# Kernel optimization log

Hardware: AMD Instinct MI355X
Metric: run time of the kernel (lower is better)

Reference implementation:

```python
import jax, jax.numpy as jnp
import numpy as np

NORM = 1.0  # normalization_factor


def _glorot(key, shape):
    fan_in, fan_out = shape
    lim = float(np.sqrt(6.0 / (fan_in + fan_out)))
    return jax.random.uniform(key, shape, jnp.float32, -lim, lim)


def setup_inputs() -> dict:
    key = jax.random.key(0)
    ks = jax.random.split(key, 12)
    B, N = 8, 2048
    latent, hidden, out_dim = 64, 128, 64
    inp = {
        "latent_features": jax.random.normal(ks[0], (B, N, latent), jnp.float32),
        "adjacency_matrix": jax.random.uniform(ks[1], (B, N, N), jnp.float32),
        "node_mask": jnp.ones((B, N, 1), jnp.float32),
        # 3 GCN layers: latent->hidden, hidden->hidden, hidden->hidden
        "W0": _glorot(ks[2], (latent, hidden)), "b0": jnp.zeros((hidden,), jnp.float32),
        "W1": _glorot(ks[3], (hidden, hidden)), "b1": jnp.zeros((hidden,), jnp.float32),
        "W2": _glorot(ks[4], (hidden, hidden)), "b2": jnp.zeros((hidden,), jnp.float32),
        # output projection hidden->out_dim
        "Wout": _glorot(ks[5], (hidden, out_dim)), "bout": jnp.zeros((out_dim,), jnp.float32),
    }
    return inp


def _gcn_layer(h, adj, W, b):
    # message transform (linear), gather+sum aggregate via dense adjacency, ReLU act
    msg = h @ W + b                      # [B,N,dout]
    agg = jnp.einsum('bij,bjd->bid', adj, msg) / NORM  # sum aggregation over neighbors
    return jax.nn.relu(agg)


def reference(latent_features, adjacency_matrix, node_mask,
              W0, b0, W1, b1, W2, b2, Wout, bout):
    h = _gcn_layer(latent_features, adjacency_matrix, W0, b0)
    h = _gcn_layer(h, adjacency_matrix, W1, b1)
    h = _gcn_layer(h, adjacency_matrix, W2, b2)
    # output projection + node mask
    return (h @ Wout + bout) * node_mask
```

## Files before the change

kernel.cpp:

```cpp
#include <hip/hip_runtime.h>
#include <hip/hip_bf16.h>


typedef __bf16 bf16;
typedef __bf16 bf16x4 __attribute__((ext_vector_type(4)));
typedef __bf16 bf16x8 __attribute__((ext_vector_type(8)));
typedef float  f32x16 __attribute__((ext_vector_type(16)));
typedef float  f32x4  __attribute__((ext_vector_type(4)));

static __device__ inline f32x16 mfma32(bf16x8 a, bf16x8 b, f32x16 c) {
    return __builtin_amdgcn_mfma_f32_32x32x16_bf16(a, b, c, 0, 0, 0);
}

static __device__ inline void tile_barrier() {
    asm volatile("s_waitcnt lgkmcnt(0)" ::: "memory");
    __builtin_amdgcn_s_barrier();
    asm volatile("" ::: "memory");
}

#define NB   8
#define NN   2048
#define LAT  64
#define HID  128
#define ODIM 64

__global__ __launch_bounds__(256) void prep_t0_k(
    const float* __restrict__ lat, const float* __restrict__ W0,
    const float* __restrict__ b0,
    const float* __restrict__ W1, const float* __restrict__ W2,
    const float* __restrict__ Wout,
    bf16* __restrict__ msgT, bf16* __restrict__ WT1,
    bf16* __restrict__ WT2, bf16* __restrict__ WoutT)
{
    __shared__ __align__(16) bf16 WTs[HID * 72];
    int tid = threadIdx.x;
    int blk = blockIdx.x;

    if (blk >= 256) {
        int i = (blk - 256) * 256 + tid;
        if (i < HID * HID) { int fo = i >> 7, k = i & 127; WT1[i] = (bf16)W1[k * HID + fo]; return; }
        i -= HID * HID;
        if (i < HID * HID) { int fo = i >> 7, k = i & 127; WT2[i] = (bf16)W2[k * HID + fo]; return; }
        i -= HID * HID;
        if (i < ODIM * HID) { int o = i >> 7, k = i & 127; WoutT[i] = (bf16)Wout[k * ODIM + o]; return; }
        return;
    }

    for (int i = tid; i < LAT * HID; i += 256) {
        int k = i >> 7, fo = i & 127;
        WTs[fo * 72 + k] = (bf16)W0[i];
    }
    __syncthreads();

    int l = tid & 63, w = tid >> 6;
    int lm = l & 31, lh = l >> 5;
    int g0 = blk * 64;
    int b  = g0 >> 11, nb = g0 & 2047;

    const bf16*  Wrow = &WTs[(w * 32 + lm) * 72 + lh * 8];
    const float* r0   = lat + (size_t)(g0 + lm) * LAT + lh * 8;
    const float* r1   = r0 + (size_t)32 * LAT;

    f32x16 acc0 = {}, acc1 = {};
#pragma unroll
    for (int k0 = 0; k0 < LAT; k0 += 16) {
        bf16x8 a = *(const bf16x8*)(Wrow + k0);
        f32x4 x0 = *(const f32x4*)(r0 + k0), x1 = *(const f32x4*)(r0 + k0 + 4);
        f32x4 y0 = *(const f32x4*)(r1 + k0), y1 = *(const f32x4*)(r1 + k0 + 4);
        bf16x8 v0, v1;
        v0[0]=(bf16)x0[0]; v0[1]=(bf16)x0[1]; v0[2]=(bf16)x0[2]; v0[3]=(bf16)x0[3];
        v0[4]=(bf16)x1[0]; v0[5]=(bf16)x1[1]; v0[6]=(bf16)x1[2]; v0[7]=(bf16)x1[3];
        v1[0]=(bf16)y0[0]; v1[1]=(bf16)y0[1]; v1[2]=(bf16)y0[2]; v1[3]=(bf16)y0[3];
        v1[4]=(bf16)y1[0]; v1[5]=(bf16)y1[1]; v1[6]=(bf16)y1[2]; v1[7]=(bf16)y1[3];
        acc0 = mfma32(a, v0, acc0);
        acc1 = mfma32(a, v1, acc1);
    }

    bf16* outb = msgT + (size_t)b * (HID * NN) + nb;
#pragma unroll
    for (int r = 0; r < 16; ++r) {
        int fo = w * 32 + (r & 3) + 8 * (r >> 2) + 4 * lh;
        float bv = b0[fo];
        outb[(size_t)fo * NN + lm]      = (bf16)(acc0[r] + bv);
        outb[(size_t)fo * NN + 32 + lm] = (bf16)(acc1[r] + bv);
    }
}

template<int MODE, int ADJW>
__global__ __launch_bounds__(256) void agg_k(
    const float* __restrict__ adjf, const bf16* __restrict__ adjbi,
    bf16* __restrict__ adjbo,
    const bf16* __restrict__ msgT, const bf16* __restrict__ WTn,
    const float* __restrict__ biasn, bf16* __restrict__ msg_out,
    const float* __restrict__ mask, float* __restrict__ out)
{
    __shared__ __align__(16) bf16 As[2][32 * 72];
    __shared__ __align__(16) bf16 Bs[2][128 * 72];
    __shared__ __align__(16) bf16 Hs[32 * 136];
    int tid = threadIdx.x;
    int l = tid & 63, w = tid >> 6;
    int lm = l & 31, lh = l >> 5;
    int b  = blockIdx.x & 7;
    int m0 = (blockIdx.x >> 3) * 32;

    const bf16* msgb = msgT + (size_t)b * (HID * NN);
    int br = tid >> 3, bc = (tid & 7) * 8;
    const bf16* bsrc = msgb + (size_t)br * NN + bc;

    int ar = tid >> 4, ac = (tid & 15) * 4;
    const float* asrc = (ADJW == 0) ? adjf + (size_t)b * NN * NN + (size_t)(m0 + ar) * NN + ac : nullptr;
    bf16* adst = (ADJW == 0) ? adjbo + (size_t)b * NN * NN + (size_t)(m0 + ar) * NN + ac : nullptr;
    int ar8 = tid >> 3, ac8 = (tid & 7) * 8;
    const bf16* asrcb = (ADJW == 1) ? adjbi + (size_t)b * NN * NN + (size_t)(m0 + ar8) * NN + ac8 : nullptr;

    f32x4  fa0[2], fa1[2];
    bf16x8 ba[2];
    bf16x8 pb[2][4];

    auto loadTile = [&](int set, int k) {
        if (ADJW == 0) {
            fa0[set] = *(const f32x4*)(asrc + k);
            fa1[set] = *(const f32x4*)(asrc + (size_t)16 * NN + k);
        } else {
            ba[set] = *(const bf16x8*)(asrcb + k);
        }
        pb[set][0] = *(const bf16x8*)(bsrc + k);
        pb[set][1] = *(const bf16x8*)(bsrc + (size_t)32 * NN + k);
        pb[set][2] = *(const bf16x8*)(bsrc + (size_t)64 * NN + k);
        pb[set][3] = *(const bf16x8*)(bsrc + (size_t)96 * NN + k);
    };
    auto storeTile = [&](int set, int buf, int k) {
        if (ADJW == 0) {
            bf16x4 v0, v1;
            v0[0]=(bf16)fa0[set][0]; v0[1]=(bf16)fa0[set][1]; v0[2]=(bf16)fa0[set][2]; v0[3]=(bf16)fa0[set][3];
            v1[0]=(bf16)fa1[set][0]; v1[1]=(bf16)fa1[set][1]; v1[2]=(bf16)fa1[set][2]; v1[3]=(bf16)fa1[set][3];
            *(bf16x4*)&As[buf][ar * 72 + ac]        = v0;
            *(bf16x4*)&As[buf][(ar + 16) * 72 + ac] = v1;
            *(bf16x4*)(adst + k)                    = v0;
            *(bf16x4*)(adst + (size_t)16 * NN + k)  = v1;
        } else {
            *(bf16x8*)&As[buf][ar8 * 72 + ac8] = ba[set];
        }
        *(bf16x8*)&Bs[buf][br * 72 + bc]        = pb[set][0];
        *(bf16x8*)&Bs[buf][(br + 32) * 72 + bc] = pb[set][1];
        *(bf16x8*)&Bs[buf][(br + 64) * 72 + bc] = pb[set][2];
        *(bf16x8*)&Bs[buf][(br + 96) * 72 + bc] = pb[set][3];
    };

    f32x16 acc = {};
    auto mfmaTile = [&](int buf) {
        const bf16* Ac = &As[buf][lm * 72 + lh * 8];
        const bf16* Bc = &Bs[buf][(w * 32 + lm) * 72 + lh * 8];
#pragma unroll
        for (int s = 0; s < 4; ++s)
            acc = mfma32(*(const bf16x8*)(Ac + s * 16), *(const bf16x8*)(Bc + s * 16), acc);
    };

    loadTile(0, 0);
    loadTile(1, 64);
    storeTile(0, 0, 0);
    tile_barrier();

#pragma unroll 1
    for (int kt = 0; kt < 32; kt += 2) {
        if (kt + 2 < 32) loadTile(0, (kt + 2) * 64);
        mfmaTile(0);
        storeTile(1, 1, (kt + 1) * 64);
        tile_barrier();
        if (kt + 3 < 32) loadTile(1, (kt + 3) * 64);
        mfmaTile(1);
        if (kt + 2 < 32) storeTile(0, 0, (kt + 2) * 64);
        tile_barrier();
    }

#pragma unroll
    for (int r = 0; r < 16; ++r) {
        int row = (r & 3) + 8 * (r >> 2) + 4 * lh;
        float v = acc[r];
        Hs[row * 136 + w * 32 + lm] = (bf16)(v > 0.f ? v : 0.f);
    }
    __syncthreads();

    if (MODE == 0) {
        const bf16* Arow = WTn + (size_t)(w * 32 + lm) * HID + lh * 8;
        const bf16* Brow = &Hs[lm * 136 + lh * 8];
        f32x16 acc2 = {};
#pragma unroll
        for (int s = 0; s < 8; ++s)
            acc2 = mfma32(*(const bf16x8*)(Arow + s * 16), *(const bf16x8*)(Brow + s * 16), acc2);
        bf16* outb = msg_out + (size_t)b * (HID * NN) + m0;
#pragma unroll
        for (int r = 0; r < 16; ++r) {
            int fo = w * 32 + (r & 3) + 8 * (r >> 2) + 4 * lh;
            outb[(size_t)fo * NN + lm] = (bf16)(acc2[r] + biasn[fo]);
        }
    } else {
        if (w < 2) {
            int ob = w * 32;
            const bf16* Arow = &Hs[lm * 136 + lh * 8];
            const bf16* Brow = WTn + (size_t)(ob + lm) * HID + lh * 8;
            f32x16 acc2 = {};
#pragma unroll
            for (int s = 0; s < 8; ++s)
                acc2 = mfma32(*(const bf16x8*)(Arow + s * 16), *(const bf16x8*)(Brow + s * 16), acc2);
            float bv = biasn[ob + lm];
#pragma unroll
            for (int r = 0; r < 16; ++r) {
                int node = (r & 3) + 8 * (r >> 2) + 4 * lh;
                int g = b * NN + m0 + node;
                out[(size_t)g * ODIM + ob + lm] = (acc2[r] + bv) * mask[g];
            }
        }
    }
}

extern "C" void kernel_launch(void* const* d_in, const int* in_sizes, int n_in,
                              void* d_out, int out_size, void* d_ws, size_t ws_size,
                              hipStream_t stream)
{
    const float* lat  = (const float*)d_in[0];
    const float* adj  = (const float*)d_in[1];
    const float* mask = (const float*)d_in[2];
    const float* W0   = (const float*)d_in[3];
    const float* b0   = (const float*)d_in[4];
    const float* W1   = (const float*)d_in[5];
    const float* b1   = (const float*)d_in[6];
    const float* W2   = (const float*)d_in[7];
    const float* b2   = (const float*)d_in[8];
    const float* Wout = (const float*)d_in[9];
    const float* bout = (const float*)d_in[10];
    float* out = (float*)d_out;

    char* ws = (char*)d_ws;
    bf16* msgA  = (bf16*)(ws + 0);
    bf16* msgB  = (bf16*)(ws + 4194304);
    bf16* adjbf = (bf16*)(ws + 8388608);
    bf16* WT1   = (bf16*)(ws + 75497472);
    bf16* WT2   = (bf16*)(ws + 75530240);
    bf16* WoutT = (bf16*)(ws + 75563008);

    prep_t0_k<<<416, 256, 0, stream>>>(lat, W0, b0, W1, W2, Wout, msgA, WT1, WT2, WoutT);

    agg_k<0, 0><<<512, 256, 0, stream>>>(adj, nullptr, adjbf, msgA, WT1, b1, msgB, nullptr, nullptr);
    agg_k<0, 1><<<512, 256, 0, stream>>>(nullptr, adjbf, nullptr, msgB, WT2, b2, msgA, nullptr, nullptr);
    agg_k<1, 1><<<512, 256, 0, stream>>>(nullptr, adjbf, nullptr, msgA, WoutT, bout, nullptr, mask, out);
}
```

Before: 284.8 us.

## Enlarge aggregation tiles to 64 rows and 128-deep K with 512-thread blocks

The aggregation kernel now processes 64 output rows per block instead of 32, and takes a K step of 128 instead of 64. It runs 8 waves arranged 2x4 over 256 blocks. This halves how often the msg matrix is re-read from global memory per row block and halves the number of barriers. The store for the next tile is now issued before the MFMAs rather than after. The trade-off is larger LDS use (about 87KB) and fewer blocks than CUs, which could leave some compute units idle.

```diff
diff --git a/kernel.cpp b/kernel.cpp
--- a/kernel.cpp
+++ b/kernel.cpp
@@ -23,6 +23,10 @@
 #define LAT  64
 #define HID  128
 #define ODIM 64
+#define BM   64
+#define BK   128
+#define NP   16
+#define LDK  136
 
 __global__ __launch_bounds__(256) void prep_t0_k(
     const float* __restrict__ lat, const float* __restrict__ W0,
@@ -87,117 +91,128 @@
 }
 
 template<int MODE, int ADJW>
-__global__ __launch_bounds__(256) void agg_k(
+__global__ __launch_bounds__(512) void agg_k(
     const float* __restrict__ adjf, const bf16* __restrict__ adjbi,
     bf16* __restrict__ adjbo,
     const bf16* __restrict__ msgT, const bf16* __restrict__ WTn,
     const float* __restrict__ biasn, bf16* __restrict__ msg_out,
     const float* __restrict__ mask, float* __restrict__ out)
 {
-    __shared__ __align__(16) bf16 As[2][32 * 72];
-    __shared__ __align__(16) bf16 Bs[2][128 * 72];
-    __shared__ __align__(16) bf16 Hs[32 * 136];
+    __shared__ __align__(16) bf16 As[2][BM * LDK];
+    __shared__ __align__(16) bf16 Bs[2][HID * LDK];
+    __shared__ __align__(16) bf16 Hs[BM * LDK];
     int tid = threadIdx.x;
     int l = tid & 63, w = tid >> 6;
     int lm = l & 31, lh = l >> 5;
+    int wm = w >> 2, wn = w & 3;
     int b  = blockIdx.x & 7;
-    int m0 = (blockIdx.x >> 3) * 32;
+    int m0 = (blockIdx.x >> 3) * BM;
 
     const bf16* msgb = msgT + (size_t)b * (HID * NN);
-    int br = tid >> 3, bc = (tid & 7) * 8;
-    const bf16* bsrc = msgb + (size_t)br * NN + bc;
-
-    int ar = tid >> 4, ac = (tid & 15) * 4;
-    const float* asrc = (ADJW == 0) ? adjf + (size_t)b * NN * NN + (size_t)(m0 + ar) * NN + ac : nullptr;
-    bf16* adst = (ADJW == 0) ? adjbo + (size_t)b * NN * NN + (size_t)(m0 + ar) * NN + ac : nullptr;
-    int ar8 = tid >> 3, ac8 = (tid & 7) * 8;
-    const bf16* asrcb = (ADJW == 1) ? adjbi + (size_t)b * NN * NN + (size_t)(m0 + ar8) * NN + ac8 : nullptr;
-
-    f32x4  fa0[2], fa1[2];
-    bf16x8 ba[2];
+    int br = tid >> 3, bc8 = (tid & 7) * 8;
+    const bf16* bsrc = msgb + (size_t)br * NN + bc8;
+
+    int ar = tid >> 3, acf = (tid & 7) * 4;
+    const float* asrc = (ADJW == 0) ? adjf + (size_t)b * NN * NN + (size_t)(m0 + ar) * NN + acf : nullptr;
+    bf16* adst = (ADJW == 0) ? adjbo + (size_t)b * NN * NN + (size_t)(m0 + ar) * NN + acf : nullptr;
+    int ac8 = (tid & 7) * 8;
+    const bf16* asrcb = (ADJW == 1) ? adjbi + (size_t)b * NN * NN + (size_t)(m0 + ar) * NN + ac8 : nullptr;
+
+    f32x4  fa[2][4];
+    bf16x8 ba[2][2];
     bf16x8 pb[2][4];
 
     auto loadTile = [&](int set, int k) {
         if (ADJW == 0) {
-            fa0[set] = *(const f32x4*)(asrc + k);
-            fa1[set] = *(const f32x4*)(asrc + (size_t)16 * NN + k);
+#pragma unroll
+            for (int g = 0; g < 4; ++g) fa[set][g] = *(const f32x4*)(asrc + k + g * 32);
         } else {
-            ba[set] = *(const bf16x8*)(asrcb + k);
-        }
-        pb[set][0] = *(const bf16x8*)(bsrc + k);
-        pb[set][1] = *(const bf16x8*)(bsrc + (size_t)32 * NN + k);
-        pb[set][2] = *(const bf16x8*)(bsrc + (size_t)64 * NN + k);
-        pb[set][3] = *(const bf16x8*)(bsrc + (size_t)96 * NN + k);
+#pragma unroll
+            for (int g = 0; g < 2; ++g) ba[set][g] = *(const bf16x8*)(asrcb + k + g * 64);
+        }
+#pragma unroll
+        for (int h = 0; h < 2; ++h)
+#pragma unroll
+            for (int g = 0; g < 2; ++g)
+                pb[set][h * 2 + g] = *(const bf16x8*)(bsrc + (size_t)(h * 64) * NN + k + g * 64);
     };
     auto storeTile = [&](int set, int buf, int k) {
         if (ADJW == 0) {
-            bf16x4 v0, v1;
-            v0[0]=(bf16)fa0[set][0]; v0[1]=(bf16)fa0[set][1]; v0[2]=(bf16)fa0[set][2]; v0[3]=(bf16)fa0[set][3];
-            v1[0]=(bf16)fa1[set][0]; v1[1]=(bf16)fa1[set][1]; v1[2]=(bf16)fa1[set][2]; v1[3]=(bf16)fa1[set][3];
-            *(bf16x4*)&As[buf][ar * 72 + ac]        = v0;
-            *(bf16x4*)&As[buf][(ar + 16) * 72 + ac] = v1;
-            *(bf16x4*)(adst + k)                    = v0;
-            *(bf16x4*)(adst + (size_t)16 * NN + k)  = v1;
+#pragma unroll
+            for (int g = 0; g < 4; ++g) {
+                bf16x4 v;
+                v[0]=(bf16)fa[set][g][0]; v[1]=(bf16)fa[set][g][1];
+                v[2]=(bf16)fa[set][g][2]; v[3]=(bf16)fa[set][g][3];
+                *(bf16x4*)&As[buf][ar * LDK + acf + g * 32] = v;
+                *(bf16x4*)(adst + k + g * 32)               = v;
+            }
         } else {
-            *(bf16x8*)&As[buf][ar8 * 72 + ac8] = ba[set];
-        }
-        *(bf16x8*)&Bs[buf][br * 72 + bc]        = pb[set][0];
-        *(bf16x8*)&Bs[buf][(br + 32) * 72 + bc] = pb[set][1];
-        *(bf16x8*)&Bs[buf][(br + 64) * 72 + bc] = pb[set][2];
-        *(bf16x8*)&Bs[buf][(br + 96) * 72 + bc] = pb[set][3];
+#pragma unroll
+            for (int g = 0; g < 2; ++g)
+                *(bf16x8*)&As[buf][ar * LDK + ac8 + g * 64] = ba[set][g];
+        }
+#pragma unroll
+        for (int h = 0; h < 2; ++h)
+#pragma unroll
+            for (int g = 0; g < 2; ++g)
+                *(bf16x8*)&Bs[buf][(br + h * 64) * LDK + bc8 + g * 64] = pb[set][h * 2 + g];
     };
 
     f32x16 acc = {};
     auto mfmaTile = [&](int buf) {
-        const bf16* Ac = &As[buf][lm * 72 + lh * 8];
-        const bf16* Bc = &Bs[buf][(w * 32 + lm) * 72 + lh * 8];
-#pragma unroll
-        for (int s = 0; s < 4; ++s)
+        const bf16* Ac = &As[buf][(wm * 32 + lm) * LDK + lh * 8];
+        const bf16* Bc = &Bs[buf][(wn * 32 + lm) * LDK + lh * 8];
+#pragma unroll
+        for (int s = 0; s < 8; ++s)
             acc = mfma32(*(const bf16x8*)(Ac + s * 16), *(const bf16x8*)(Bc + s * 16), acc);
     };
 
-    loadTile(0, 0);
-    loadTile(1, 64);
-    storeTile(0, 0, 0);
+    loadTile(0, 0 * BK);
+    loadTile(1, 1 * BK);
+    storeTile(0, 0, 0 * BK);
     tile_barrier();
 
+#define PHASE(U)                                                               \
+    do {                                                                       \
+        int q = qb + (U);                                                      \
+        if (q + 2 < NP) loadTile((U), (q + 2) * BK);                           \
+        if (q + 1 < NP) storeTile(((U) + 1) & 1, ((U) + 1) & 1, (q + 1) * BK); \
+        mfmaTile((U) & 1);                                                     \
+        tile_barrier();                                                        \
+    } while (0)
+
 #pragma unroll 1
-    for (int kt = 0; kt < 32; kt += 2) {
-        if (kt + 2 < 32) loadTile(0, (kt + 2) * 64);
-        mfmaTile(0);
-        storeTile(1, 1, (kt + 1) * 64);
-        tile_barrier();
-        if (kt + 3 < 32) loadTile(1, (kt + 3) * 64);
-        mfmaTile(1);
-        if (kt + 2 < 32) storeTile(0, 0, (kt + 2) * 64);
-        tile_barrier();
-    }
+    for (int qb = 0; qb < NP; qb += 2) {
+        PHASE(0);
+        PHASE(1);
+    }
+#undef PHASE
 
 #pragma unroll
     for (int r = 0; r < 16; ++r) {
-        int row = (r & 3) + 8 * (r >> 2) + 4 * lh;
+        int row = wm * 32 + (r & 3) + 8 * (r >> 2) + 4 * lh;
         float v = acc[r];
-        Hs[row * 136 + w * 32 + lm] = (bf16)(v > 0.f ? v : 0.f);
+        Hs[row * LDK + wn * 32 + lm] = (bf16)(v > 0.f ? v : 0.f);
     }
     __syncthreads();
 
     if (MODE == 0) {
-        const bf16* Arow = WTn + (size_t)(w * 32 + lm) * HID + lh * 8;
-        const bf16* Brow = &Hs[lm * 136 + lh * 8];
+        const bf16* Arow = WTn + (size_t)(wn * 32 + lm) * HID + lh * 8;
+        const bf16* Brow = &Hs[(wm * 32 + lm) * LDK + lh * 8];
         f32x16 acc2 = {};
 #pragma unroll
         for (int s = 0; s < 8; ++s)
             acc2 = mfma32(*(const bf16x8*)(Arow + s * 16), *(const bf16x8*)(Brow + s * 16), acc2);
-        bf16* outb = msg_out + (size_t)b * (HID * NN) + m0;
+        bf16* outb = msg_out + (size_t)b * (HID * NN) + m0 + wm * 32;
 #pragma unroll
         for (int r = 0; r < 16; ++r) {
-            int fo = w * 32 + (r & 3) + 8 * (r >> 2) + 4 * lh;
+            int fo = wn * 32 + (r & 3) + 8 * (r >> 2) + 4 * lh;
             outb[(size_t)fo * NN + lm] = (bf16)(acc2[r] + biasn[fo]);
         }
     } else {
-        if (w < 2) {
-            int ob = w * 32;
-            const bf16* Arow = &Hs[lm * 136 + lh * 8];
+        if (wn < 2) {
+            int ob = wn * 32;
+            const bf16* Arow = &Hs[(wm * 32 + lm) * LDK + lh * 8];
             const bf16* Brow = WTn + (size_t)(ob + lm) * HID + lh * 8;
             f32x16 acc2 = {};
 #pragma unroll
@@ -206,7 +221,7 @@
             float bv = biasn[ob + lm];
 #pragma unroll
             for (int r = 0; r < 16; ++r) {
-                int node = (r & 3) + 8 * (r >> 2) + 4 * lh;
+                int node = wm * 32 + (r & 3) + 8 * (r >> 2) + 4 * lh;
                 int g = b * NN + m0 + node;
                 out[(size_t)g * ODIM + ob + lm] = (acc2[r] + bv) * mask[g];
             }
@@ -241,7 +256,7 @@
 
     prep_t0_k<<<416, 256, 0, stream>>>(lat, W0, b0, W1, W2, Wout, msgA, WT1, WT2, WoutT);
 
-    agg_k<0, 0><<<512, 256, 0, stream>>>(adj, nullptr, adjbf, msgA, WT1, b1, msgB, nullptr, nullptr);
-    agg_k<0, 1><<<512, 256, 0, stream>>>(nullptr, adjbf, nullptr, msgB, WT2, b2, msgA, nullptr, nullptr);
-    agg_k<1, 1><<<512, 256, 0, stream>>>(nullptr, adjbf, nullptr, msgA, WoutT, bout, nullptr, mask, out);
-}
+    agg_k<0, 0><<<256, 512, 0, stream>>>(adj, nullptr, adjbf, msgA, WT1, b1, msgB, nullptr, nullptr);
+    agg_k<0, 1><<<256, 512, 0, stream>>>(nullptr, adjbf, nullptr, msgB, WT2, b2, msgA, nullptr, nullptr);
+    agg_k<1, 1><<<256, 512, 0, stream>>>(nullptr, adjbf, nullptr, msgA, WoutT, bout, nullptr, mask, out);
+}
```

Result: faster. 267.8 us (-6.0%).
